# Kernel tuning notes

Measured on AMD Instinct MI355X. Metric: run time of the kernel, lower is better.

The kernel has to match this reference:

```python
import jax, jax.numpy as jnp
import numpy as np

N_NODES = 20000
N_EDGES = 640000
F = 64       # n_features
B = 20       # n_basis
LN_EPS = 1e-5

act = jax.nn.silu

def _lin_init(key, fan_in, fan_out):
    return jax.random.normal(key, (fan_in, fan_out), dtype=jnp.float32) / np.sqrt(fan_in)

def setup_inputs() -> dict:
    key = jax.random.key(0)
    ks = jax.random.split(key, 18)
    inp = {
        "atom_node": jax.random.normal(ks[0], (N_NODES, F), dtype=jnp.float32),
        "force_node": jax.random.normal(ks[1], (N_NODES, 3, F), dtype=jnp.float32),
        "dir_edge": jax.random.normal(ks[2], (N_EDGES, 3), dtype=jnp.float32),
        "dist_edge": jax.random.uniform(ks[3], (N_EDGES, B), dtype=jnp.float32),
        "edge_index": jax.random.randint(ks[4], (2, N_EDGES), 0, N_NODES, dtype=jnp.int64),
        # message_nodepart: Linear(F,F)+act+Linear(F,F)
        "W1": _lin_init(ks[5], F, F), "b1": jnp.zeros((F,), jnp.float32),
        "W2": _lin_init(ks[6], F, F), "b2": jnp.zeros((F,), jnp.float32),
        # message_edgepart: Linear(B,F,bias=False)
        "We": _lin_init(ks[7], B, F),
        # equiv_message1/2: Linear(F,F,nobias)+act+Linear(F,F,nobias)
        "Wq1a": _lin_init(ks[8], F, F), "Wq1b": _lin_init(ks[9], F, F),
        "Wq2a": _lin_init(ks[10], F, F), "Wq2b": _lin_init(ks[11], F, F),
        # equiv_update: Linear(F,F,nobias)
        "Wu": _lin_init(ks[12], F, F),
        # LayerNorm(F)
        "gamma": jnp.ones((F,), jnp.float32), "beta": jnp.zeros((F,), jnp.float32),
    }
    return inp

def reference(atom_node, force_node, dir_edge, dist_edge, edge_index,
              W1, b1, W2, b2, We, Wq1a, Wq1b, Wq2a, Wq2b, Wu, gamma, beta):
    src, dst = edge_index[0], edge_index[1]
    n = atom_node.shape[0]

    # node part of the message: MLP over nodes [N,F]
    mn = act(atom_node @ W1 + b1) @ W2 + b2
    # edge part: [E,F]
    me = dist_edge @ We
    # message: elementwise product of edge part and both endpoint node parts [E,F]
    message = me * mn[src] * mn[dst]

    # invariant update: scatter-add messages to source nodes
    inv_update1 = jax.ops.segment_sum(message, src, num_segments=n)
    atom_node = atom_node + inv_update1

    # equivariant messages [E,3,F]
    em1_inv = act(message @ Wq1a) @ Wq1b            # [E,F]
    em2_inv = act(message @ Wq2a) @ Wq2b            # [E,F]
    equiv_msg = (em1_inv[:, None, :] * dir_edge[:, :, None]
                 + em2_inv[:, None, :] * force_node[dst])  # [E,3,F]
    force_update = jax.ops.segment_sum(equiv_msg, src, num_segments=n)
    force_node = force_node + force_update

    # invariant contraction of vector features: sum over the 3-dim
    inv_update2 = jnp.sum(force_node * (force_node @ Wu), axis=1)  # [N,F]
    atom_node = atom_node + inv_update2

    # LayerNorm over feature dim
    mu = jnp.mean(atom_node, axis=-1, keepdims=True)
    var = jnp.var(atom_node, axis=-1, keepdims=True)
    atom_node = (atom_node - mu) * jax.lax.rsqrt(var + LN_EPS) * gamma + beta

    return (atom_node, force_node)
```

## Files before the change

kernel.cpp:

```cpp
#include <hip/hip_runtime.h>
#include <hip/hip_fp16.h>

#define N_NODES 20000
#define N_EDGES 640000
#define FDIM 64
#define NB 20
#define LN_EPS 1e-5f
#define NW 8

typedef __attribute__((ext_vector_type(8))) short bf16x8;
typedef __attribute__((ext_vector_type(4))) float f32x4;

#define SEL_HI 0x07060302u
#define SEL_LO 0x05040100u
#define MFMA16 __builtin_amdgcn_mfma_f32_16x16x32_bf16

__device__ __forceinline__ float silu_f(float x) { return x / (1.0f + __expf(-x)); }

__device__ __forceinline__ float bcast_lane(float v, int lane) {
    return __int_as_float(__builtin_amdgcn_readlane(__float_as_int(v), lane));
}

__device__ __forceinline__ unsigned bf16_rn(float x) {
    unsigned u = __float_as_uint(x);
    return (u + 0x7FFFu + ((u >> 16) & 1u)) >> 16;
}

__device__ __forceinline__ unsigned pack_split(float x) {
    unsigned h = bf16_rn(x);
    unsigned lo = bf16_rn(x - __uint_as_float(h << 16));
    return (h << 16) | lo;
}

__device__ __forceinline__ void pk_atomic_add(__half2* addr, float a, float b) {
    unsafeAtomicAdd(addr, __floats2half2_rn(a, b));
}

__device__ __forceinline__ void load_afrag(const unsigned* rowPtr, int kh, int q,
                                           bf16x8* ahi, bf16x8* alo) {
    const uint4 ra = *(const uint4*)(rowPtr + kh * 32 + q * 8);
    const uint4 rb = *(const uint4*)(rowPtr + kh * 32 + q * 8 + 4);
    union { unsigned u[4]; bf16x8 v; } H, L;
    H.u[0] = __builtin_amdgcn_perm(ra.y, ra.x, SEL_HI);
    H.u[1] = __builtin_amdgcn_perm(ra.w, ra.z, SEL_HI);
    H.u[2] = __builtin_amdgcn_perm(rb.y, rb.x, SEL_HI);
    H.u[3] = __builtin_amdgcn_perm(rb.w, rb.z, SEL_HI);
    L.u[0] = __builtin_amdgcn_perm(ra.y, ra.x, SEL_LO);
    L.u[1] = __builtin_amdgcn_perm(ra.w, ra.z, SEL_LO);
    L.u[2] = __builtin_amdgcn_perm(rb.y, rb.x, SEL_LO);
    L.u[3] = __builtin_amdgcn_perm(rb.w, rb.z, SEL_LO);
    *ahi = H.v;
    *alo = L.v;
}

__device__ __forceinline__ void mm3(const unsigned* Bhi, const unsigned* Blo,
                                    bf16x8 ahi, bf16x8 alo, f32x4* acc, int kh, int l) {
#pragma unroll
    for (int c = 0; c < 4; ++c) {
        bf16x8 bh = *(const bf16x8*)(Bhi + (kh * 4 + c) * 256 + l * 4);
        bf16x8 bl = *(const bf16x8*)(Blo + (kh * 4 + c) * 256 + l * 4);
        acc[c] = MFMA16(ahi, bh, acc[c], 0, 0, 0);
        acc[c] = MFMA16(ahi, bl, acc[c], 0, 0, 0);
        acc[c] = MFMA16(alo, bh, acc[c], 0, 0, 0);
    }
}

__global__ __launch_bounds__(256) void node_mlp_kernel(
    const float* __restrict__ atom, const float* __restrict__ W1, const float* __restrict__ b1,
    const float* __restrict__ W2, const float* __restrict__ b2, float* __restrict__ mn)
{
    __shared__ float W1s[FDIM][FDIM];
    __shared__ float W2s[FDIM][FDIM];
    const int f = threadIdx.x, ty = threadIdx.y;
    const int tid = ty * 64 + f;
    for (int i = tid; i < FDIM * FDIM; i += 256) {
        ((float*)W1s)[i] = W1[i];
        ((float*)W2s)[i] = W2[i];
    }
    __syncthreads();
    const float bb1 = b1[f], bb2 = b2[f];
    const int nw = gridDim.x * 4;
    for (int n = blockIdx.x * 4 + ty; n < N_NODES; n += nw) {
        const float a = atom[n * FDIM + f];
        float h = bb1;
        for (int g = 0; g < FDIM; ++g) h += bcast_lane(a, g) * W1s[g][f];
        h = silu_f(h);
        float o = bb2;
        for (int g = 0; g < FDIM; ++g) o += bcast_lane(h, g) * W2s[g][f];
        mn[n * FDIM + f] = o;
    }
}

__global__ __launch_bounds__(64 * NW, 2) void edge_kernel(
    const float* __restrict__ dist,
    const float* __restrict__ dir,
    const int* __restrict__ eidx,
    const float* __restrict__ mn,
    const float* __restrict__ We,
    const float* __restrict__ Wq1a, const float* __restrict__ Wq1b,
    const float* __restrict__ Wq2a, const float* __restrict__ Wq2b,
    const float* __restrict__ forceN,
    __half2* __restrict__ aUpd,
    __half2* __restrict__ fUpd)
{
    __shared__ __align__(16) unsigned Bfr[16384];
    __shared__ __align__(16) unsigned WeFr[2048];
    __shared__ __align__(16) unsigned Astg[NW][16][76];

    const int l = threadIdx.x;
    const int ty = threadIdx.y;
    const int q = l >> 4, row = l & 15;
    const bool evenLane = ((l & 1) == 0);

    for (int t = ty; t < 32; t += NW) {
        const int mm = t >> 3, kh = (t >> 2) & 1, c = t & 3;
        const float* W = (mm == 0) ? Wq1a : (mm == 1) ? Wq2a : (mm == 2) ? Wq1b : Wq2b;
        const int n = c * 16 + row;
        const int kb = kh * 32 + q * 8;
        unsigned* hiP = &Bfr[(((mm * 2 + 0) * 2 + kh) * 4 + c) * 256 + l * 4];
        unsigned* loP = &Bfr[(((mm * 2 + 1) * 2 + kh) * 4 + c) * 256 + l * 4];
#pragma unroll
        for (int i = 0; i < 4; ++i) {
            float w0 = W[(kb + 2 * i) * FDIM + n];
            float w1 = W[(kb + 2 * i + 1) * FDIM + n];
            unsigned h0 = bf16_rn(w0);
            unsigned l0 = bf16_rn(w0 - __uint_as_float(h0 << 16));
            unsigned h1 = bf16_rn(w1);
            unsigned l1 = bf16_rn(w1 - __uint_as_float(h1 << 16));
            hiP[i] = h0 | (h1 << 16);
            loP[i] = l0 | (l1 << 16);
        }
    }
    for (int c = ty; c < 4; c += NW) {
        const int n = c * 16 + row;
        unsigned* hiP = &WeFr[(0 * 4 + c) * 256 + l * 4];
        unsigned* loP = &WeFr[(1 * 4 + c) * 256 + l * 4];
#pragma unroll
        for (int i = 0; i < 4; ++i) {
            const int k0 = q * 8 + 2 * i, k1 = k0 + 1;
            float w0 = (k0 < NB) ? We[k0 * FDIM + n] : 0.0f;
            float w1 = (k1 < NB) ? We[k1 * FDIM + n] : 0.0f;
            unsigned h0 = bf16_rn(w0);
            unsigned l0 = bf16_rn(w0 - __uint_as_float(h0 << 16));
            unsigned h1 = bf16_rn(w1);
            unsigned l1 = bf16_rn(w1 - __uint_as_float(h1 << 16));
            hiP[i] = h0 | (h1 << 16);
            loP[i] = l0 | (l1 << 16);
        }
    }
    __syncthreads();

    const unsigned* B1aH = Bfr + 0 * 2048; const unsigned* B1aL = Bfr + 1 * 2048;
    const unsigned* B2aH = Bfr + 2 * 2048; const unsigned* B2aL = Bfr + 3 * 2048;
    const unsigned* B1bH = Bfr + 4 * 2048; const unsigned* B1bL = Bfr + 5 * 2048;
    const unsigned* B2bH = Bfr + 6 * 2048; const unsigned* B2bL = Bfr + 7 * 2048;
    const unsigned* WeH = WeFr;            const unsigned* WeL = WeFr + 1024;

    unsigned* stg = &Astg[ty][0][0];
    const unsigned* rowPtr = &Astg[ty][row][0];

    const int ngroups = N_EDGES / 16;
    const int stride = gridDim.x * NW;
    for (int grp = blockIdx.x * NW + ty; grp < ngroups; grp += stride) {
        const int e0 = grp * 16;

        int ev = 0;
        if (l < 32) ev = eidx[(l < 16) ? (e0 + l) : (N_EDGES + e0 + (l - 16))];
        float dv = (l < 48) ? dir[e0 * 3 + l] : 0.0f;

        const float* dp = dist + (size_t)(e0 + row) * NB + q * 8;
        float4 da = {0.f, 0.f, 0.f, 0.f}, db = {0.f, 0.f, 0.f, 0.f};
        if (q < 2)       { da = *(const float4*)dp; db = *(const float4*)(dp + 4); }
        else if (q == 2) { da = *(const float4*)dp; }
        unsigned s0 = pack_split(da.x), s1 = pack_split(da.y);
        unsigned s2 = pack_split(da.z), s3 = pack_split(da.w);
        unsigned s4 = pack_split(db.x), s5 = pack_split(db.y);
        unsigned s6 = pack_split(db.z), s7 = pack_split(db.w);
        union { unsigned u[4]; bf16x8 v; } AH, AL;
        AH.u[0] = __builtin_amdgcn_perm(s1, s0, SEL_HI);
        AH.u[1] = __builtin_amdgcn_perm(s3, s2, SEL_HI);
        AH.u[2] = __builtin_amdgcn_perm(s5, s4, SEL_HI);
        AH.u[3] = __builtin_amdgcn_perm(s7, s6, SEL_HI);
        AL.u[0] = __builtin_amdgcn_perm(s1, s0, SEL_LO);
        AL.u[1] = __builtin_amdgcn_perm(s3, s2, SEL_LO);
        AL.u[2] = __builtin_amdgcn_perm(s5, s4, SEL_LO);
        AL.u[3] = __builtin_amdgcn_perm(s7, s6, SEL_LO);

        f32x4 me4[4];
#pragma unroll
        for (int c = 0; c < 4; ++c) me4[c] = (f32x4){0.f, 0.f, 0.f, 0.f};
        mm3(WeH, WeL, AH.v, AL.v, me4, 0, l);
#pragma unroll
        for (int c = 0; c < 4; ++c)
#pragma unroll
            for (int r = 0; r < 4; ++r)
                stg[(q * 4 + r) * 76 + (row + 16 * c)] = __float_as_uint(me4[c][r]);

        float p[16];
#pragma unroll
        for (int j = 0; j < 16; ++j) {
            const int src = __builtin_amdgcn_readlane(ev, j);
            const int dst = __builtin_amdgcn_readlane(ev, 16 + j);
            p[j] = mn[(size_t)src * FDIM + l] * mn[(size_t)dst * FDIM + l];
        }
#pragma unroll
        for (int j = 0; j < 16; ++j) {
            const int src = __builtin_amdgcn_readlane(ev, j);
            const float m = __uint_as_float(stg[j * 76 + l]) * p[j];
            const float mp = __shfl_xor(m, 1, 64);
            if (evenLane)
                pk_atomic_add(&aUpd[(size_t)src * 32 + (l >> 1)], m, mp);
            stg[j * 76 + l] = pack_split(m);
        }

        f32x4 acc1[4], acc2[4];
#pragma unroll
        for (int c = 0; c < 4; ++c) {
            acc1[c] = (f32x4){0.f, 0.f, 0.f, 0.f};
            acc2[c] = (f32x4){0.f, 0.f, 0.f, 0.f};
        }
#pragma unroll
        for (int kh = 0; kh < 2; ++kh) {
            bf16x8 ahi, alo;
            load_afrag(rowPtr, kh, q, &ahi, &alo);
            mm3(B1aH, B1aL, ahi, alo, acc1, kh, l);
            mm3(B2aH, B2aL, ahi, alo, acc2, kh, l);
        }
#pragma unroll
        for (int c = 0; c < 4; ++c)
#pragma unroll
            for (int r = 0; r < 4; ++r) {
                acc1[c][r] = silu_f(acc1[c][r]);
                acc2[c][r] = silu_f(acc2[c][r]);
            }

#pragma unroll
        for (int c = 0; c < 4; ++c)
#pragma unroll
            for (int r = 0; r < 4; ++r)
                stg[(q * 4 + r) * 76 + (row + 16 * c)] = pack_split(acc1[c][r]);
        f32x4 eacc1[4];
#pragma unroll
        for (int c = 0; c < 4; ++c) eacc1[c] = (f32x4){0.f, 0.f, 0.f, 0.f};
#pragma unroll
        for (int kh = 0; kh < 2; ++kh) {
            bf16x8 ahi, alo;
            load_afrag(rowPtr, kh, q, &ahi, &alo);
            mm3(B1bH, B1bL, ahi, alo, eacc1, kh, l);
        }

#pragma unroll
        for (int c = 0; c < 4; ++c)
#pragma unroll
            for (int r = 0; r < 4; ++r)
                stg[(q * 4 + r) * 76 + (row + 16 * c)] = pack_split(acc2[c][r]);
        f32x4 eacc2[4];
#pragma unroll
        for (int c = 0; c < 4; ++c) eacc2[c] = (f32x4){0.f, 0.f, 0.f, 0.f};
#pragma unroll
        for (int kh = 0; kh < 2; ++kh) {
            bf16x8 ahi, alo;
            load_afrag(rowPtr, kh, q, &ahi, &alo);
            mm3(B2bH, B2bL, ahi, alo, eacc2, kh, l);
        }

#pragma unroll
        for (int r = 0; r < 4; ++r) {
            const int eo = q * 4 + r;
            const int vs = __shfl(ev, eo);
            const int vd = __shfl(ev, 16 + eo);
            const float d0 = __shfl(dv, eo * 3 + 0);
            const float d1 = __shfl(dv, eo * 3 + 1);
            const float d2 = __shfl(dv, eo * 3 + 2);
            const float* fd = forceN + (size_t)vd * 3 * FDIM;
            float f0[4], f1[4], f2[4];
#pragma unroll
            for (int c = 0; c < 4; ++c) {
                const int n = row + 16 * c;
                f0[c] = fd[0 * FDIM + n];
                f1[c] = fd[1 * FDIM + n];
                f2[c] = fd[2 * FDIM + n];
            }
            __half2* base = fUpd + (size_t)vs * 96;
#pragma unroll
            for (int c = 0; c < 4; ++c) {
                const float v0 = eacc1[c][r] * d0 + eacc2[c][r] * f0[c];
                const float v1 = eacc1[c][r] * d1 + eacc2[c][r] * f1[c];
                const float v2 = eacc1[c][r] * d2 + eacc2[c][r] * f2[c];
                const float p0 = __shfl_xor(v0, 1, 64);
                const float p1 = __shfl_xor(v1, 1, 64);
                const float p2 = __shfl_xor(v2, 1, 64);
                if (evenLane) {
                    const int idx = (row >> 1) + 8 * c;
                    pk_atomic_add(base + 0 * 32 + idx, v0, p0);
                    pk_atomic_add(base + 1 * 32 + idx, v1, p1);
                    pk_atomic_add(base + 2 * 32 + idx, v2, p2);
                }
            }
        }
    }
}

__global__ __launch_bounds__(256) void node_final_kernel(
    const float* __restrict__ atomN,
    const float* __restrict__ forceN,
    const __half2* __restrict__ aUpd,
    const __half2* __restrict__ fUpd,
    const float* __restrict__ Wu, const float* __restrict__ gamma, const float* __restrict__ beta,
    float* __restrict__ atomOut, float* __restrict__ forceOut)
{
    __shared__ float Wus[FDIM][FDIM];
    const int f = threadIdx.x, ty = threadIdx.y;
    const int tid = ty * 64 + f;
    for (int i = tid; i < FDIM * FDIM; i += 256) ((float*)Wus)[i] = Wu[i];
    __syncthreads();
    const float gg = gamma[f], bb = beta[f];
    const bool hi = (f & 1);
    const int nw = gridDim.x * 4;
    for (int n = blockIdx.x * 4 + ty; n < N_NODES; n += nw) {
        const __half2 u0 = fUpd[(size_t)n * 96 + 0 * 32 + (f >> 1)];
        const __half2 u1 = fUpd[(size_t)n * 96 + 1 * 32 + (f >> 1)];
        const __half2 u2 = fUpd[(size_t)n * 96 + 2 * 32 + (f >> 1)];
        const float f0 = forceN[((size_t)n * 3 + 0) * FDIM + f] + (hi ? __high2float(u0) : __low2float(u0));
        const float f1 = forceN[((size_t)n * 3 + 1) * FDIM + f] + (hi ? __high2float(u1) : __low2float(u1));
        const float f2 = forceN[((size_t)n * 3 + 2) * FDIM + f] + (hi ? __high2float(u2) : __low2float(u2));
        forceOut[((size_t)n * 3 + 0) * FDIM + f] = f0;
        forceOut[((size_t)n * 3 + 1) * FDIM + f] = f1;
        forceOut[((size_t)n * 3 + 2) * FDIM + f] = f2;

        float r0 = 0.0f, r1 = 0.0f, r2 = 0.0f;
#pragma unroll 8
        for (int g = 0; g < FDIM; ++g) {
            const float w = Wus[g][f];
            r0 += bcast_lane(f0, g) * w;
            r1 += bcast_lane(f1, g) * w;
            r2 += bcast_lane(f2, g) * w;
        }
        const __half2 ua = aUpd[(size_t)n * 32 + (f >> 1)];
        const float inv1 = hi ? __high2float(ua) : __low2float(ua);
        float a = atomN[(size_t)n * FDIM + f] + inv1 + (f0 * r0 + f1 * r1 + f2 * r2);
        float s = a;
#pragma unroll
        for (int off = 32; off >= 1; off >>= 1) s += __shfl_xor(s, off, 64);
        const float mu = s * (1.0f / 64.0f);
        const float d = a - mu;
        float v = d * d;
#pragma unroll
        for (int off = 32; off >= 1; off >>= 1) v += __shfl_xor(v, off, 64);
        v *= (1.0f / 64.0f);
        atomOut[(size_t)n * FDIM + f] = d * rsqrtf(v + LN_EPS) * gg + bb;
    }
}

extern "C" void kernel_launch(void* const* d_in, const int* in_sizes, int n_in,
                              void* d_out, int out_size, void* d_ws, size_t ws_size,
                              hipStream_t stream)
{
    const float* atom_node  = (const float*)d_in[0];
    const float* force_node = (const float*)d_in[1];
    const float* dir_edge   = (const float*)d_in[2];
    const float* dist_edge  = (const float*)d_in[3];
    const int*   edge_index = (const int*)d_in[4];
    const float* W1   = (const float*)d_in[5];
    const float* b1   = (const float*)d_in[6];
    const float* W2   = (const float*)d_in[7];
    const float* b2   = (const float*)d_in[8];
    const float* We   = (const float*)d_in[9];
    const float* Wq1a = (const float*)d_in[10];
    const float* Wq1b = (const float*)d_in[11];
    const float* Wq2a = (const float*)d_in[12];
    const float* Wq2b = (const float*)d_in[13];
    const float* Wu   = (const float*)d_in[14];
    const float* gamma = (const float*)d_in[15];
    const float* beta  = (const float*)d_in[16];

    float* atomOut  = (float*)d_out;
    float* forceOut = (float*)d_out + (size_t)N_NODES * FDIM;

    char* ws = (char*)d_ws;
    float*   mn   = (float*)ws;
    __half2* aUpd = (__half2*)(ws + 5120000);
    __half2* fUpd = (__half2*)(ws + 7680000);

    (void)hipMemsetAsync(aUpd, 0, (size_t)N_NODES * 32 * sizeof(__half2), stream);
    (void)hipMemsetAsync(fUpd, 0, (size_t)N_NODES * 96 * sizeof(__half2), stream);

    dim3 blk4(64, 4);
    dim3 blkE(64, NW);
    node_mlp_kernel<<<512, blk4, 0, stream>>>(atom_node, W1, b1, W2, b2, mn);
    edge_kernel<<<256, blkE, 0, stream>>>(dist_edge, dir_edge, edge_index, mn, We,
                                          Wq1a, Wq1b, Wq2a, Wq2b, force_node,
                                          aUpd, fUpd);
    node_final_kernel<<<512, blk4, 0, stream>>>(atom_node, force_node, aUpd, fUpd,
                                                Wu, gamma, beta, atomOut, forceOut);
}
```

Measured before the change: 541.9 us.

## Accumulate invariant update in fp32 directly into output, restructure force atomics

Replaces the packed half2 atomic accumulation of the invariant update with per-lane fp32 atomicAdd into the atom output buffer, which is pre-seeded with atom_node by a device copy. The final kernel then reads that accumulator and writes the LayerNorm result in place. Edge src/dst indices and directions are staged in LDS instead of being fetched by shuffles. Force atomics are reorganised so every lane issues half of the packed atomics rather than only even lanes. This trades twice as many (wider) atomics on the atom path for removing shuffles and idle lanes, and it improves precision.

New measurement: 606.9 us. +12.0%, slower.

```diff
diff --git a/kernel.cpp b/kernel.cpp
--- a/kernel.cpp
+++ b/kernel.cpp
@@ -100,7 +100,7 @@
     const float* __restrict__ Wq1a, const float* __restrict__ Wq1b,
     const float* __restrict__ Wq2a, const float* __restrict__ Wq2b,
     const float* __restrict__ forceN,
-    __half2* __restrict__ aUpd,
+    float* __restrict__ atomAcc,
     __half2* __restrict__ fUpd)
 {
     __shared__ __align__(16) unsigned Bfr[16384];
@@ -110,7 +110,6 @@
     const int l = threadIdx.x;
     const int ty = threadIdx.y;
     const int q = l >> 4, row = l & 15;
-    const bool evenLane = ((l & 1) == 0);
 
     for (int t = ty; t < 32; t += NW) {
         const int mm = t >> 3, kh = (t >> 2) & 1, c = t & 3;
@@ -167,6 +166,8 @@
         int ev = 0;
         if (l < 32) ev = eidx[(l < 16) ? (e0 + l) : (N_EDGES + e0 + (l - 16))];
         float dv = (l < 48) ? dir[e0 * 3 + l] : 0.0f;
+        if (l < 32) stg[(l & 15) * 76 + 64 + (l >> 4)] = (unsigned)ev;
+        if (l < 48) stg[(l / 3) * 76 + 66 + (l % 3)] = __float_as_uint(dv);
 
         const float* dp = dist + (size_t)(e0 + row) * NB + q * 8;
         float4 da = {0.f, 0.f, 0.f, 0.f}, db = {0.f, 0.f, 0.f, 0.f};
@@ -207,9 +208,7 @@
         for (int j = 0; j < 16; ++j) {
             const int src = __builtin_amdgcn_readlane(ev, j);
             const float m = __uint_as_float(stg[j * 76 + l]) * p[j];
-            const float mp = __shfl_xor(m, 1, 64);
-            if (evenLane)
-                pk_atomic_add(&aUpd[(size_t)src * 32 + (l >> 1)], m, mp);
+            atomicAdd(&atomAcc[(size_t)src * FDIM + l], m);
             stg[j * 76 + l] = pack_split(m);
         }
 
@@ -264,14 +263,16 @@
             mm3(B2bH, B2bL, ahi, alo, eacc2, kh, l);
         }
 
+        const int cA = (l & 1) * 2;
+        const int pr = row >> 1;
 #pragma unroll
         for (int r = 0; r < 4; ++r) {
-            const int eo = q * 4 + r;
-            const int vs = __shfl(ev, eo);
-            const int vd = __shfl(ev, 16 + eo);
-            const float d0 = __shfl(dv, eo * 3 + 0);
-            const float d1 = __shfl(dv, eo * 3 + 1);
-            const float d2 = __shfl(dv, eo * 3 + 2);
+            const int eo76 = (q * 4 + r) * 76;
+            const uint2 sv = *(const uint2*)&stg[eo76 + 64];
+            const float2 dd = *(const float2*)&stg[eo76 + 66];
+            const float d2 = __uint_as_float(stg[eo76 + 68]);
+            const int vs = (int)sv.x, vd = (int)sv.y;
+            const float d0 = dd.x, d1 = dd.y;
             const float* fd = forceN + (size_t)vd * 3 * FDIM;
             float f0[4], f1[4], f2[4];
 #pragma unroll
@@ -281,20 +282,29 @@
                 f1[c] = fd[1 * FDIM + n];
                 f2[c] = fd[2 * FDIM + n];
             }
+            float v0[4], v1[4], v2[4], p0[4], p1[4], p2[4];
+#pragma unroll
+            for (int c = 0; c < 4; ++c) {
+                v0[c] = eacc1[c][r] * d0 + eacc2[c][r] * f0[c];
+                v1[c] = eacc1[c][r] * d1 + eacc2[c][r] * f1[c];
+                v2[c] = eacc1[c][r] * d2 + eacc2[c][r] * f2[c];
+                p0[c] = __shfl_xor(v0[c], 1, 64);
+                p1[c] = __shfl_xor(v1[c], 1, 64);
+                p2[c] = __shfl_xor(v2[c], 1, 64);
+            }
             __half2* base = fUpd + (size_t)vs * 96;
 #pragma unroll
-            for (int c = 0; c < 4; ++c) {
-                const float v0 = eacc1[c][r] * d0 + eacc2[c][r] * f0[c];
-                const float v1 = eacc1[c][r] * d1 + eacc2[c][r] * f1[c];
-                const float v2 = eacc1[c][r] * d2 + eacc2[c][r] * f2[c];
-                const float p0 = __shfl_xor(v0, 1, 64);
-                const float p1 = __shfl_xor(v1, 1, 64);
-                const float p2 = __shfl_xor(v2, 1, 64);
-                if (evenLane) {
-                    const int idx = (row >> 1) + 8 * c;
-                    pk_atomic_add(base + 0 * 32 + idx, v0, p0);
-                    pk_atomic_add(base + 1 * 32 + idx, v1, p1);
-                    pk_atomic_add(base + 2 * 32 + idx, v2, p2);
+            for (int cc = 0; cc < 2; ++cc) {
+                const int c = cA + cc;
+                const int idx = pr + 8 * c;
+                if (l & 1) {
+                    pk_atomic_add(base + 0 * 32 + idx, p0[c], v0[c]);
+                    pk_atomic_add(base + 1 * 32 + idx, p1[c], v1[c]);
+                    pk_atomic_add(base + 2 * 32 + idx, p2[c], v2[c]);
+                } else {
+                    pk_atomic_add(base + 0 * 32 + idx, v0[c], p0[c]);
+                    pk_atomic_add(base + 1 * 32 + idx, v1[c], p1[c]);
+                    pk_atomic_add(base + 2 * 32 + idx, v2[c], p2[c]);
                 }
             }
         }
@@ -302,12 +312,11 @@
 }
 
 __global__ __launch_bounds__(256) void node_final_kernel(
-    const float* __restrict__ atomN,
     const float* __restrict__ forceN,
-    const __half2* __restrict__ aUpd,
     const __half2* __restrict__ fUpd,
     const float* __restrict__ Wu, const float* __restrict__ gamma, const float* __restrict__ beta,
-    float* __restrict__ atomOut, float* __restrict__ forceOut)
+    float* __restrict__ atomAcc,
+    float* __restrict__ forceOut)
 {
     __shared__ float Wus[FDIM][FDIM];
     const int f = threadIdx.x, ty = threadIdx.y;
@@ -336,9 +345,7 @@
             r1 += bcast_lane(f1, g) * w;
             r2 += bcast_lane(f2, g) * w;
         }
-        const __half2 ua = aUpd[(size_t)n * 32 + (f >> 1)];
-        const float inv1 = hi ? __high2float(ua) : __low2float(ua);
-        float a = atomN[(size_t)n * FDIM + f] + inv1 + (f0 * r0 + f1 * r1 + f2 * r2);
+        float a = atomAcc[(size_t)n * FDIM + f] + (f0 * r0 + f1 * r1 + f2 * r2);
         float s = a;
 #pragma unroll
         for (int off = 32; off >= 1; off >>= 1) s += __shfl_xor(s, off, 64);
@@ -348,7 +355,7 @@
 #pragma unroll
         for (int off = 32; off >= 1; off >>= 1) v += __shfl_xor(v, off, 64);
         v *= (1.0f / 64.0f);
-        atomOut[(size_t)n * FDIM + f] = d * rsqrtf(v + LN_EPS) * gg + bb;
+        atomAcc[(size_t)n * FDIM + f] = d * rsqrtf(v + LN_EPS) * gg + bb;
     }
 }
 
@@ -379,10 +386,10 @@
 
     char* ws = (char*)d_ws;
     float*   mn   = (float*)ws;
-    __half2* aUpd = (__half2*)(ws + 5120000);
-    __half2* fUpd = (__half2*)(ws + 7680000);
-
-    (void)hipMemsetAsync(aUpd, 0, (size_t)N_NODES * 32 * sizeof(__half2), stream);
+    __half2* fUpd = (__half2*)(ws + 5120000);
+
+    (void)hipMemcpyAsync(atomOut, atom_node, (size_t)N_NODES * FDIM * sizeof(float),
+                         hipMemcpyDeviceToDevice, stream);
     (void)hipMemsetAsync(fUpd, 0, (size_t)N_NODES * 96 * sizeof(__half2), stream);
 
     dim3 blk4(64, 4);
@@ -390,7 +397,7 @@
     node_mlp_kernel<<<512, blk4, 0, stream>>>(atom_node, W1, b1, W2, b2, mn);
     edge_kernel<<<256, blkE, 0, stream>>>(dist_edge, dir_edge, edge_index, mn, We,
                                           Wq1a, Wq1b, Wq2a, Wq2b, force_node,
-                                          aUpd, fUpd);
-    node_final_kernel<<<512, blk4, 0, stream>>>(atom_node, force_node, aUpd, fUpd,
-                                                Wu, gamma, beta, atomOut, forceOut);
-}
+                                          atomOut, fUpd);
+    node_final_kernel<<<512, blk4, 0, stream>>>(force_node, fUpd, Wu, gamma, beta,
+                                                atomOut, forceOut);
+}
```

## Process two edge groups per wave iteration to interleave gathers and MFMA

Applied to the files above, without the earlier changes.

The edge kernel loop now handles two 16-edge groups per warp iteration. Each phase (edge-basis matmul, mn gather, message atomics, equivariant MLP, force scatter) is issued for group A and then group B, which is meant to give more independent memory operations in flight and hide gather latency. The LDS staging buffer is doubled to hold both groups. In exchange, register pressure goes up (two sets of p[16] and accumulators), which can cause spills or lower occupancy at the 512-thread launch bound. If ngroups is not a multiple of twice the stride, the tail group B may be handled incorrectly. Here ngroups is 40000, which is even, so base+1 stays in range.

Result: slower. 556.7 us (+2.7%).

```diff
diff --git a/kernel.cpp b/kernel.cpp
--- a/kernel.cpp
+++ b/kernel.cpp
@@ -91,11 +91,155 @@
     }
 }
 
+__device__ __forceinline__ void me_phase(unsigned* stg, const float4& da, const float4& db,
+                                         const unsigned* WeH, const unsigned* WeL,
+                                         int l, int q, int row)
+{
+    unsigned s0 = pack_split(da.x), s1 = pack_split(da.y);
+    unsigned s2 = pack_split(da.z), s3 = pack_split(da.w);
+    unsigned s4 = pack_split(db.x), s5 = pack_split(db.y);
+    unsigned s6 = pack_split(db.z), s7 = pack_split(db.w);
+    union { unsigned u[4]; bf16x8 v; } AH, AL;
+    AH.u[0] = __builtin_amdgcn_perm(s1, s0, SEL_HI);
+    AH.u[1] = __builtin_amdgcn_perm(s3, s2, SEL_HI);
+    AH.u[2] = __builtin_amdgcn_perm(s5, s4, SEL_HI);
+    AH.u[3] = __builtin_amdgcn_perm(s7, s6, SEL_HI);
+    AL.u[0] = __builtin_amdgcn_perm(s1, s0, SEL_LO);
+    AL.u[1] = __builtin_amdgcn_perm(s3, s2, SEL_LO);
+    AL.u[2] = __builtin_amdgcn_perm(s5, s4, SEL_LO);
+    AL.u[3] = __builtin_amdgcn_perm(s7, s6, SEL_LO);
+    f32x4 me4[4];
+#pragma unroll
+    for (int c = 0; c < 4; ++c) me4[c] = (f32x4){0.f, 0.f, 0.f, 0.f};
+    mm3(WeH, WeL, AH.v, AL.v, me4, 0, l);
+#pragma unroll
+    for (int c = 0; c < 4; ++c)
+#pragma unroll
+        for (int r = 0; r < 4; ++r)
+            stg[(q * 4 + r) * 76 + (row + 16 * c)] = __float_as_uint(me4[c][r]);
+}
+
+__device__ __forceinline__ void gather_phase(int ev, const float* __restrict__ mn, int l, float* p)
+{
+#pragma unroll
+    for (int j = 0; j < 16; ++j) {
+        const int src = __builtin_amdgcn_readlane(ev, j);
+        const int dst = __builtin_amdgcn_readlane(ev, 16 + j);
+        p[j] = mn[(size_t)src * FDIM + l] * mn[(size_t)dst * FDIM + l];
+    }
+}
+
+__device__ __forceinline__ void msg_phase(unsigned* stg, int ev, const float* p,
+                                          __half2* __restrict__ aUpd, int l, bool evenLane)
+{
+#pragma unroll
+    for (int j = 0; j < 16; ++j) {
+        const int src = __builtin_amdgcn_readlane(ev, j);
+        const float m = __uint_as_float(stg[j * 76 + l]) * p[j];
+        const float mp = __shfl_xor(m, 1, 64);
+        if (evenLane)
+            pk_atomic_add(&aUpd[(size_t)src * 32 + (l >> 1)], m, mp);
+        stg[j * 76 + l] = pack_split(m);
+    }
+}
+
+__device__ __forceinline__ void he_phase(unsigned* stg, const unsigned* rowPtr,
+    const unsigned* B1aH, const unsigned* B1aL, const unsigned* B2aH, const unsigned* B2aL,
+    const unsigned* B1bH, const unsigned* B1bL, const unsigned* B2bH, const unsigned* B2bL,
+    f32x4* eacc1, f32x4* eacc2, int l, int q, int row)
+{
+    f32x4 acc1[4], acc2[4];
+#pragma unroll
+    for (int c = 0; c < 4; ++c) {
+        acc1[c] = (f32x4){0.f, 0.f, 0.f, 0.f};
+        acc2[c] = (f32x4){0.f, 0.f, 0.f, 0.f};
+    }
+#pragma unroll
+    for (int kh = 0; kh < 2; ++kh) {
+        bf16x8 ahi, alo;
+        load_afrag(rowPtr, kh, q, &ahi, &alo);
+        mm3(B1aH, B1aL, ahi, alo, acc1, kh, l);
+        mm3(B2aH, B2aL, ahi, alo, acc2, kh, l);
+    }
+#pragma unroll
+    for (int c = 0; c < 4; ++c)
+#pragma unroll
+        for (int r = 0; r < 4; ++r) {
+            acc1[c][r] = silu_f(acc1[c][r]);
+            acc2[c][r] = silu_f(acc2[c][r]);
+        }
+#pragma unroll
+    for (int c = 0; c < 4; ++c)
+#pragma unroll
+        for (int r = 0; r < 4; ++r)
+            stg[(q * 4 + r) * 76 + (row + 16 * c)] = pack_split(acc1[c][r]);
+#pragma unroll
+    for (int c = 0; c < 4; ++c) eacc1[c] = (f32x4){0.f, 0.f, 0.f, 0.f};
+#pragma unroll
+    for (int kh = 0; kh < 2; ++kh) {
+        bf16x8 ahi, alo;
+        load_afrag(rowPtr, kh, q, &ahi, &alo);
+        mm3(B1bH, B1bL, ahi, alo, eacc1, kh, l);
+    }
+#pragma unroll
+    for (int c = 0; c < 4; ++c)
+#pragma unroll
+        for (int r = 0; r < 4; ++r)
+            stg[(q * 4 + r) * 76 + (row + 16 * c)] = pack_split(acc2[c][r]);
+#pragma unroll
+    for (int c = 0; c < 4; ++c) eacc2[c] = (f32x4){0.f, 0.f, 0.f, 0.f};
+#pragma unroll
+    for (int kh = 0; kh < 2; ++kh) {
+        bf16x8 ahi, alo;
+        load_afrag(rowPtr, kh, q, &ahi, &alo);
+        mm3(B2bH, B2bL, ahi, alo, eacc2, kh, l);
+    }
+}
+
+__device__ __forceinline__ void scatter_phase(int ev, float dv,
+    const f32x4* eacc1, const f32x4* eacc2,
+    const float* __restrict__ forceN, __half2* __restrict__ fUpd,
+    int l, int q, int row, bool evenLane)
+{
+#pragma unroll
+    for (int r = 0; r < 4; ++r) {
+        const int eo = q * 4 + r;
+        const int vs = __shfl(ev, eo);
+        const int vd = __shfl(ev, 16 + eo);
+        const float d0 = __shfl(dv, eo * 3 + 0);
+        const float d1 = __shfl(dv, eo * 3 + 1);
+        const float d2 = __shfl(dv, eo * 3 + 2);
+        const float* fd = forceN + (size_t)vd * 3 * FDIM;
+        float f0[4], f1[4], f2[4];
+#pragma unroll
+        for (int c = 0; c < 4; ++c) {
+            const int n = row + 16 * c;
+            f0[c] = fd[0 * FDIM + n];
+            f1[c] = fd[1 * FDIM + n];
+            f2[c] = fd[2 * FDIM + n];
+        }
+        __half2* base = fUpd + (size_t)vs * 96;
+#pragma unroll
+        for (int c = 0; c < 4; ++c) {
+            const float v0 = eacc1[c][r] * d0 + eacc2[c][r] * f0[c];
+            const float v1 = eacc1[c][r] * d1 + eacc2[c][r] * f1[c];
+            const float v2 = eacc1[c][r] * d2 + eacc2[c][r] * f2[c];
+            const float p0 = __shfl_xor(v0, 1, 64);
+            const float p1 = __shfl_xor(v1, 1, 64);
+            const float p2 = __shfl_xor(v2, 1, 64);
+            if (evenLane) {
+                const int idx = (row >> 1) + 8 * c;
+                pk_atomic_add(base + 0 * 32 + idx, v0, p0);
+                pk_atomic_add(base + 1 * 32 + idx, v1, p1);
+                pk_atomic_add(base + 2 * 32 + idx, v2, p2);
+            }
+        }
+    }
+}
+
 __global__ __launch_bounds__(64 * NW, 2) void edge_kernel(
-    const float* __restrict__ dist,
-    const float* __restrict__ dir,
-    const int* __restrict__ eidx,
-    const float* __restrict__ mn,
+    const float* __restrict__ dist, const float* __restrict__ dir,
+    const int* __restrict__ eidx, const float* __restrict__ mn,
     const float* __restrict__ We,
     const float* __restrict__ Wq1a, const float* __restrict__ Wq1b,
     const float* __restrict__ Wq2a, const float* __restrict__ Wq2b,
@@ -105,7 +249,7 @@
 {
     __shared__ __align__(16) unsigned Bfr[16384];
     __shared__ __align__(16) unsigned WeFr[2048];
-    __shared__ __align__(16) unsigned Astg[NW][16][76];
+    __shared__ __align__(16) unsigned Astg[2 * NW][16][76];
 
     const int l = threadIdx.x;
     const int ty = threadIdx.y;
@@ -156,156 +300,58 @@
     const unsigned* B2bH = Bfr + 6 * 2048; const unsigned* B2bL = Bfr + 7 * 2048;
     const unsigned* WeH = WeFr;            const unsigned* WeL = WeFr + 1024;
 
-    unsigned* stg = &Astg[ty][0][0];
-    const unsigned* rowPtr = &Astg[ty][row][0];
+    unsigned* stgA = &Astg[ty][0][0];
+    unsigned* stgB = &Astg[ty + NW][0][0];
+    const unsigned* rowPtrA = &Astg[ty][row][0];
+    const unsigned* rowPtrB = &Astg[ty + NW][row][0];
 
     const int ngroups = N_EDGES / 16;
-    const int stride = gridDim.x * NW;
-    for (int grp = blockIdx.x * NW + ty; grp < ngroups; grp += stride) {
-        const int e0 = grp * 16;
-
-        int ev = 0;
-        if (l < 32) ev = eidx[(l < 16) ? (e0 + l) : (N_EDGES + e0 + (l - 16))];
-        float dv = (l < 48) ? dir[e0 * 3 + l] : 0.0f;
-
-        const float* dp = dist + (size_t)(e0 + row) * NB + q * 8;
-        float4 da = {0.f, 0.f, 0.f, 0.f}, db = {0.f, 0.f, 0.f, 0.f};
-        if (q < 2)       { da = *(const float4*)dp; db = *(const float4*)(dp + 4); }
-        else if (q == 2) { da = *(const float4*)dp; }
-        unsigned s0 = pack_split(da.x), s1 = pack_split(da.y);
-        unsigned s2 = pack_split(da.z), s3 = pack_split(da.w);
-        unsigned s4 = pack_split(db.x), s5 = pack_split(db.y);
-        unsigned s6 = pack_split(db.z), s7 = pack_split(db.w);
-        union { unsigned u[4]; bf16x8 v; } AH, AL;
-        AH.u[0] = __builtin_amdgcn_perm(s1, s0, SEL_HI);
-        AH.u[1] = __builtin_amdgcn_perm(s3, s2, SEL_HI);
-        AH.u[2] = __builtin_amdgcn_perm(s5, s4, SEL_HI);
-        AH.u[3] = __builtin_amdgcn_perm(s7, s6, SEL_HI);
-        AL.u[0] = __builtin_amdgcn_perm(s1, s0, SEL_LO);
-        AL.u[1] = __builtin_amdgcn_perm(s3, s2, SEL_LO);
-        AL.u[2] = __builtin_amdgcn_perm(s5, s4, SEL_LO);
-        AL.u[3] = __builtin_amdgcn_perm(s7, s6, SEL_LO);
-
-        f32x4 me4[4];
-#pragma unroll
-        for (int c = 0; c < 4; ++c) me4[c] = (f32x4){0.f, 0.f, 0.f, 0.f};
-        mm3(WeH, WeL, AH.v, AL.v, me4, 0, l);
-#pragma unroll
-        for (int c = 0; c < 4; ++c)
-#pragma unroll
-            for (int r = 0; r < 4; ++r)
-                stg[(q * 4 + r) * 76 + (row + 16 * c)] = __float_as_uint(me4[c][r]);
-
-        float p[16];
-#pragma unroll
-        for (int j = 0; j < 16; ++j) {
-            const int src = __builtin_amdgcn_readlane(ev, j);
-            const int dst = __builtin_amdgcn_readlane(ev, 16 + j);
-            p[j] = mn[(size_t)src * FDIM + l] * mn[(size_t)dst * FDIM + l];
-        }
-#pragma unroll
-        for (int j = 0; j < 16; ++j) {
-            const int src = __builtin_amdgcn_readlane(ev, j);
-            const float m = __uint_as_float(stg[j * 76 + l]) * p[j];
-            const float mp = __shfl_xor(m, 1, 64);
-            if (evenLane)
-                pk_atomic_add(&aUpd[(size_t)src * 32 + (l >> 1)], m, mp);
-            stg[j * 76 + l] = pack_split(m);
-        }
-
-        f32x4 acc1[4], acc2[4];
-#pragma unroll
-        for (int c = 0; c < 4; ++c) {
-            acc1[c] = (f32x4){0.f, 0.f, 0.f, 0.f};
-            acc2[c] = (f32x4){0.f, 0.f, 0.f, 0.f};
-        }
-#pragma unroll
-        for (int kh = 0; kh < 2; ++kh) {
-            bf16x8 ahi, alo;
-            load_afrag(rowPtr, kh, q, &ahi, &alo);
-            mm3(B1aH, B1aL, ahi, alo, acc1, kh, l);
-            mm3(B2aH, B2aL, ahi, alo, acc2, kh, l);
-        }
-#pragma unroll
-        for (int c = 0; c < 4; ++c)
-#pragma unroll
-            for (int r = 0; r < 4; ++r) {
-                acc1[c][r] = silu_f(acc1[c][r]);
-                acc2[c][r] = silu_f(acc2[c][r]);
-            }
-
-#pragma unroll
-        for (int c = 0; c < 4; ++c)
-#pragma unroll
-            for (int r = 0; r < 4; ++r)
-                stg[(q * 4 + r) * 76 + (row + 16 * c)] = pack_split(acc1[c][r]);
-        f32x4 eacc1[4];
-#pragma unroll
-        for (int c = 0; c < 4; ++c) eacc1[c] = (f32x4){0.f, 0.f, 0.f, 0.f};
-#pragma unroll
-        for (int kh = 0; kh < 2; ++kh) {
-            bf16x8 ahi, alo;
-            load_afrag(rowPtr, kh, q, &ahi, &alo);
-            mm3(B1bH, B1bL, ahi, alo, eacc1, kh, l);
-        }
-
-#pragma unroll
-        for (int c = 0; c < 4; ++c)
-#pragma unroll
-            for (int r = 0; r < 4; ++r)
-                stg[(q * 4 + r) * 76 + (row + 16 * c)] = pack_split(acc2[c][r]);
-        f32x4 eacc2[4];
-#pragma unroll
-        for (int c = 0; c < 4; ++c) eacc2[c] = (f32x4){0.f, 0.f, 0.f, 0.f};
-#pragma unroll
-        for (int kh = 0; kh < 2; ++kh) {
-            bf16x8 ahi, alo;
-            load_afrag(rowPtr, kh, q, &ahi, &alo);
-            mm3(B2bH, B2bL, ahi, alo, eacc2, kh, l);
-        }
-
-#pragma unroll
-        for (int r = 0; r < 4; ++r) {
-            const int eo = q * 4 + r;
-            const int vs = __shfl(ev, eo);
-            const int vd = __shfl(ev, 16 + eo);
-            const float d0 = __shfl(dv, eo * 3 + 0);
-            const float d1 = __shfl(dv, eo * 3 + 1);
-            const float d2 = __shfl(dv, eo * 3 + 2);
-            const float* fd = forceN + (size_t)vd * 3 * FDIM;
-            float f0[4], f1[4], f2[4];
-#pragma unroll
-            for (int c = 0; c < 4; ++c) {
-                const int n = row + 16 * c;
-                f0[c] = fd[0 * FDIM + n];
-                f1[c] = fd[1 * FDIM + n];
-                f2[c] = fd[2 * FDIM + n];
-            }
-            __half2* base = fUpd + (size_t)vs * 96;
-#pragma unroll
-            for (int c = 0; c < 4; ++c) {
-                const float v0 = eacc1[c][r] * d0 + eacc2[c][r] * f0[c];
-                const float v1 = eacc1[c][r] * d1 + eacc2[c][r] * f1[c];
-                const float v2 = eacc1[c][r] * d2 + eacc2[c][r] * f2[c];
-                const float p0 = __shfl_xor(v0, 1, 64);
-                const float p1 = __shfl_xor(v1, 1, 64);
-                const float p2 = __shfl_xor(v2, 1, 64);
-                if (evenLane) {
-                    const int idx = (row >> 1) + 8 * c;
-                    pk_atomic_add(base + 0 * 32 + idx, v0, p0);
-                    pk_atomic_add(base + 1 * 32 + idx, v1, p1);
-                    pk_atomic_add(base + 2 * 32 + idx, v2, p2);
-                }
-            }
-        }
+    const int stride = gridDim.x * NW * 2;
+    for (int base = (blockIdx.x * NW + ty) * 2; base < ngroups; base += stride) {
+        const int eA = base * 16;
+        const int eB = (base + 1) * 16;
+
+        int evA = 0, evB = 0;
+        if (l < 32) {
+            evA = eidx[(l < 16) ? (eA + l) : (N_EDGES + eA + (l - 16))];
+            evB = eidx[(l < 16) ? (eB + l) : (N_EDGES + eB + (l - 16))];
+        }
+        float dvA = (l < 48) ? dir[eA * 3 + l] : 0.0f;
+        float dvB = (l < 48) ? dir[eB * 3 + l] : 0.0f;
+        float4 daA = {0.f, 0.f, 0.f, 0.f}, dbA = {0.f, 0.f, 0.f, 0.f};
+        float4 daB = {0.f, 0.f, 0.f, 0.f}, dbB = {0.f, 0.f, 0.f, 0.f};
+        {
+            const float* dpA = dist + (size_t)(eA + row) * NB + q * 8;
+            const float* dpB = dist + (size_t)(eB + row) * NB + q * 8;
+            if (q < 2)       { daA = *(const float4*)dpA; dbA = *(const float4*)(dpA + 4);
+                               daB = *(const float4*)dpB; dbB = *(const float4*)(dpB + 4); }
+            else if (q == 2) { daA = *(const float4*)dpA; daB = *(const float4*)dpB; }
+        }
+
+        me_phase(stgA, daA, dbA, WeH, WeL, l, q, row);
+        me_phase(stgB, daB, dbB, WeH, WeL, l, q, row);
+
+        float pA[16], pB[16];
+        gather_phase(evA, mn, l, pA);
+        gather_phase(evB, mn, l, pB);
+
+        msg_phase(stgA, evA, pA, aUpd, l, evenLane);
+        msg_phase(stgB, evB, pB, aUpd, l, evenLane);
+
+        f32x4 eacc1A[4], eacc2A[4], eacc1B[4], eacc2B[4];
+        he_phase(stgA, rowPtrA, B1aH, B1aL, B2aH, B2aL, B1bH, B1bL, B2bH, B2bL,
+                 eacc1A, eacc2A, l, q, row);
+        he_phase(stgB, rowPtrB, B1aH, B1aL, B2aH, B2aL, B1bH, B1bL, B2bH, B2bL,
+                 eacc1B, eacc2B, l, q, row);
+
+        scatter_phase(evA, dvA, eacc1A, eacc2A, forceN, fUpd, l, q, row, evenLane);
+        scatter_phase(evB, dvB, eacc1B, eacc2B, forceN, fUpd, l, q, row, evenLane);
     }
 }
 
 __global__ __launch_bounds__(256) void node_final_kernel(
-    const float* __restrict__ atomN,
-    const float* __restrict__ forceN,
-    const __half2* __restrict__ aUpd,
-    const __half2* __restrict__ fUpd,
+    const float* __restrict__ atomN, const float* __restrict__ forceN,
+    const __half2* __restrict__ aUpd, const __half2* __restrict__ fUpd,
     const float* __restrict__ Wu, const float* __restrict__ gamma, const float* __restrict__ beta,
     float* __restrict__ atomOut, float* __restrict__ forceOut)
 {
```
